# Kernel tuning notes

Hardware: AMD Instinct MI355X
Metric: run time of the kernel (lower is better)

The kernel has to match this reference:

```python
import jax, jax.numpy as jnp
import numpy as np

DIM = 1024
NUM_HEADS = 16
HEAD_DIM = DIM // NUM_HEADS


def setup_inputs() -> dict:
    key = jax.random.key(0)
    ks = jax.random.split(key, 6)
    B, N, C = 2, 2048, DIM
    s = 1.0 / np.sqrt(C)
    return {
        "x": jax.random.normal(ks[0], (B, N, C), dtype=jnp.float32),
        "Wq": jax.random.normal(ks[1], (C, C), dtype=jnp.float32) * s,
        "Wk": jax.random.normal(ks[2], (C, C), dtype=jnp.float32) * s,
        "Wv": jax.random.normal(ks[3], (C, C), dtype=jnp.float32) * s,
        "Wproj": jax.random.normal(ks[4], (C, C), dtype=jnp.float32) * s,
        "bproj": jax.random.normal(ks[5], (C,), dtype=jnp.float32) * 0.01,
    }


def reference(x, Wq, Wk, Wv, Wproj, bproj):
    B, N, C = x.shape
    H, D = NUM_HEADS, HEAD_DIM
    scale = D ** -0.5
    # Linear (torch convention: y = x @ W.T), then split heads -> [B, H, N, D]
    q = (x @ Wq.T).reshape(B, N, H, D).transpose(0, 2, 1, 3)
    k = (x @ Wk.T).reshape(B, N, H, D).transpose(0, 2, 1, 3)
    v = (x @ Wv.T).reshape(B, N, H, D).transpose(0, 2, 1, 3)
    attn = jnp.einsum("bhnd,bhmd->bhnm", q, k) * scale  # [B,H,N,N]
    attn = jax.nn.softmax(attn, axis=-1)
    out = jnp.einsum("bhnm,bhmd->bhnd", attn, v)  # [B,H,N,D]
    out = out.transpose(0, 2, 1, 3).reshape(B, N, C)
    return out @ Wproj.T + bproj
```

## Files before the change

### kernel.cpp

```cpp
#include <hip/hip_runtime.h>
#include <stdint.h>

typedef unsigned short u16;
typedef unsigned int u32;

typedef __bf16 bf16x8 __attribute__((ext_vector_type(8)));
typedef float f32x4 __attribute__((ext_vector_type(4)));

#define LOG2E_SCALE 0.18033688011112042f

static __device__ __forceinline__ u16 f2bf(float f) {
  union { float f; u32 u; } v; v.f = f;
  u32 r = v.u + 0x7fffu + ((v.u >> 16) & 1u);
  return (u16)(r >> 16);
}
static __device__ __forceinline__ u32 pk2(float a, float b) {
  return (u32)f2bf(a) | ((u32)f2bf(b) << 16);
}

static __device__ __forceinline__ void gl_lds16(const void* g, void* l) {
  __builtin_amdgcn_global_load_lds(
      (const __attribute__((address_space(1))) u32*)g,
      (__attribute__((address_space(3))) u32*)l, 16, 0, 0);
}

__global__ void cast_kernel(const float* __restrict__ x, const float* __restrict__ wq,
                            const float* __restrict__ wk, const float* __restrict__ wv,
                            const float* __restrict__ wp,
                            u16* __restrict__ xb, u16* __restrict__ wqb, u16* __restrict__ wkb,
                            u16* __restrict__ wvb, u16* __restrict__ wpb) {
  const float* src; u16* dst; int n;
  switch (blockIdx.y) {
    case 0: src = x;  dst = xb;  n = 4194304; break;
    case 1: src = wq; dst = wqb; n = 1048576; break;
    case 2: src = wk; dst = wkb; n = 1048576; break;
    case 3: src = wv; dst = wvb; n = 1048576; break;
    default: src = wp; dst = wpb; n = 1048576; break;
  }
  int i = (blockIdx.x * 256 + threadIdx.x) * 8;
  if (i >= n) return;
  float4 a = *(const float4*)(src + i);
  float4 b = *(const float4*)(src + i + 4);
  uint4 o;
  o.x = pk2(a.x, a.y); o.y = pk2(a.z, a.w);
  o.z = pk2(b.x, b.y); o.w = pk2(b.z, b.w);
  *(uint4*)(dst + i) = o;
}

__global__ __launch_bounds__(256, 3) void gemm_all(
    const u16* __restrict__ A, const u16* __restrict__ Bq, const u16* __restrict__ Bk,
    const u16* __restrict__ Bv, u16* __restrict__ oQ, u16* __restrict__ oK,
    u16* __restrict__ oVt, float* __restrict__ oP, const float* __restrict__ bias, int proj)
{
  constexpr int K = 1024;
  __shared__ u16 As[128 * 32];
  __shared__ u16 Bs[128 * 32];
  __shared__ float tbuf[4][16 * 68];

  const int tid  = threadIdx.x;
  const int lane = tid & 63;
  const int wave = tid >> 6;
  const int cl   = lane & 15;
  const int g    = lane >> 4;
  const int wm   = (wave >> 1) * 64;
  const int wn   = (wave & 1) * 64;
  const int bm   = blockIdx.y * 128;
  const int bn   = blockIdx.x * 128;
  const int z    = blockIdx.z;
  const u16* B = proj ? Bq : (z == 0 ? Bq : (z == 1 ? Bk : Bv));

  f32x4 zero4 = {0.f, 0.f, 0.f, 0.f};
  f32x4 acc[4][4];
#pragma unroll
  for (int i = 0; i < 4; i++)
#pragma unroll
    for (int j = 0; j < 4; j++) acc[i][j] = zero4;

  const int srow = tid >> 2;
  const int sch  = (tid & 3) ^ ((srow >> 1) & 3);
  const char* aG = (const char*)(A + (size_t)(bm + srow) * K) + sch * 16;
  const char* bG = (const char*)(B + (size_t)(bn + srow) * K) + sch * 16;
  char* aL = (char*)As + tid * 16;
  char* bL = (char*)Bs + tid * 16;
  const size_t rstep = (size_t)64 * K * 2;

  const int swz = (cl >> 1) & 3;

  for (int k0 = 0; k0 < K; k0 += 32) {
    gl_lds16(aG + k0 * 2, aL);
    gl_lds16(aG + rstep + k0 * 2, aL + 4096);
    gl_lds16(bG + k0 * 2, bL);
    gl_lds16(bG + rstep + k0 * 2, bL + 4096);
    __syncthreads();

    bf16x8 af[4], bf[4];
#pragma unroll
    for (int i = 0; i < 4; i++)
      af[i] = *(const bf16x8*)(As + (wm + i * 16 + cl) * 32 + ((g ^ swz) & 3) * 8);
#pragma unroll
    for (int j = 0; j < 4; j++)
      bf[j] = *(const bf16x8*)(Bs + (wn + j * 16 + cl) * 32 + ((g ^ swz) & 3) * 8);
#pragma unroll
    for (int i = 0; i < 4; i++)
#pragma unroll
      for (int j = 0; j < 4; j++)
        acc[i][j] = __builtin_amdgcn_mfma_f32_16x16x32_bf16(af[i], bf[j], acc[i][j], 0, 0, 0);
    __syncthreads();
  }

  const int rq = g * 4;
  if (proj) {
#pragma unroll
    for (int i = 0; i < 4; i++)
#pragma unroll
      for (int j = 0; j < 4; j++)
#pragma unroll
        for (int r = 0; r < 4; r++) {
          int gm = bm + wm + i * 16 + rq + r;
          int gn = bn + wn + j * 16 + cl;
          oP[(size_t)gm * 1024 + gn] = acc[i][j][r] + bias[gn];
        }
  } else if (z <= 1) {
    u16* o = z ? oK : oQ;
#pragma unroll
    for (int i = 0; i < 4; i++)
#pragma unroll
      for (int j = 0; j < 4; j++)
#pragma unroll
        for (int r = 0; r < 4; r++) {
          int gm = bm + wm + i * 16 + rq + r;
          int gn = bn + wn + j * 16 + cl;
          int b = gm >> 11, ns = gm & 2047;
          int h = gn >> 6,  d  = gn & 63;
          o[(((size_t)(b * 16 + h)) * 2048 + ns) * 64 + d] = f2bf(acc[i][j][r]);
        }
  } else {
    float* tb = tbuf[wave];
#pragma unroll
    for (int j = 0; j < 4; j++) {
      asm volatile("s_waitcnt lgkmcnt(0)" ::: "memory");
#pragma unroll
      for (int i = 0; i < 4; i++)
        *(f32x4*)(tb + cl * 68 + i * 16 + rq) = acc[i][j];
      asm volatile("s_waitcnt lgkmcnt(0)" ::: "memory");
#pragma unroll
      for (int half = 0; half < 2; half++) {
        int dd = lane >> 2, p = (lane & 3) + half * 4;
        f32x4 x0 = *(const f32x4*)(tb + dd * 68 + p * 8);
        f32x4 x1 = *(const f32x4*)(tb + dd * 68 + p * 8 + 4);
        uint4 pkd;
        pkd.x = pk2(x0[0], x0[1]); pkd.y = pk2(x0[2], x0[3]);
        pkd.z = pk2(x1[0], x1[1]); pkd.w = pk2(x1[2], x1[3]);
        int gn = bn + wn + j * 16 + dd;
        int gm = bm + wm + p * 8;
        int b = gm >> 11, nn = gm & 2047;
        int h = gn >> 6,  dl = gn & 63;
        *(uint4*)(oVt + (((size_t)(b * 16 + h)) * 64 + dl) * 2048 + nn) = pkd;
      }
    }
  }
}

__global__ __launch_bounds__(256, 2) void attn_kernel(
    const u16* __restrict__ Q, const u16* __restrict__ Km,
    const u16* __restrict__ Vt, u16* __restrict__ O)
{
  __shared__ u16 ks[128 * 64];
  __shared__ u16 ps[128 * 128];
  __shared__ u16 vs[2][64 * 128];

  const int tid  = threadIdx.x;
  const int lane = tid & 63;
  const int wave = tid >> 6;
  const int cl   = lane & 15;
  const int g    = lane >> 4;
  const int bh   = blockIdx.y;
  const int qt   = blockIdx.x;

  const char* kB = (const char*)Km + (size_t)bh * 2048 * 128;
  const char* vB = (const char*)Vt + (size_t)bh * 64 * 4096;

  const u16* qbase = Q + ((size_t)bh * 2048 + qt * 128 + wave * 32) * 64;
  bf16x8 qf[2][2];
#pragma unroll
  for (int i = 0; i < 2; i++)
#pragma unroll
    for (int h = 0; h < 2; h++)
      qf[i][h] = *(const bf16x8*)(qbase + (i * 16 + cl) * 64 + h * 32 + g * 8);

  auto stage_k = [&](int t) {
    const char* kT = kB + (size_t)t * 16384;
#pragma unroll
    for (int r = 0; r < 4; r++) {
      int c = r * 256 + tid;
      int kv = c >> 3, s = c & 7;
      gl_lds16(kT + kv * 128 + ((s ^ (kv & 7)) * 16), (char*)ks + c * 16);
    }
  };
  auto stage_v = [&](int t) {
    const char* vT = vB + (size_t)t * 256;
    char* dst = (char*)vs[t & 1];
#pragma unroll
    for (int r = 0; r < 4; r++) {
      int c = r * 256 + tid;
      int d = c >> 4, s = c & 15;
      int ch = (s & 8) | ((s ^ (d & 7)) & 7);
      gl_lds16(vT + (size_t)d * 4096 + ch * 16, dst + c * 16);
    }
  };

  stage_k(0);
  stage_v(0);

  f32x4 zero4 = {0.f, 0.f, 0.f, 0.f};
  f32x4 o_acc[2][4];
#pragma unroll
  for (int i = 0; i < 2; i++)
#pragma unroll
    for (int j = 0; j < 4; j++) o_acc[i][j] = zero4;
  float mi[2] = {-3.0e38f, -3.0e38f};
  float li[2] = {0.f, 0.f};

  for (int t = 0; t < 16; ++t) {
    __syncthreads();
    if (t < 15) stage_v(t + 1);

    f32x4 st[8][2];
#pragma unroll
    for (int j = 0; j < 8; j++) { st[j][0] = zero4; st[j][1] = zero4; }
#pragma unroll
    for (int h = 0; h < 2; h++) {
#pragma unroll
      for (int j = 0; j < 8; j++) {
        bf16x8 kf = *(const bf16x8*)(ks + (j * 16 + cl) * 64 + (((h * 4 + g) ^ (cl & 7)) & 7) * 8);
        st[j][0] = __builtin_amdgcn_mfma_f32_16x16x32_bf16(kf, qf[0][h], st[j][0], 0, 0, 0);
        st[j][1] = __builtin_amdgcn_mfma_f32_16x16x32_bf16(kf, qf[1][h], st[j][1], 0, 0, 0);
      }
    }

    float alpha[2];
#pragma unroll
    for (int i = 0; i < 2; i++) {
      float mn = -3.0e38f;
#pragma unroll
      for (int j = 0; j < 8; j++)
#pragma unroll
        for (int r = 0; r < 4; r++) mn = fmaxf(mn, st[j][i][r]);
      mn = fmaxf(mn, __shfl_xor(mn, 16, 64));
      mn = fmaxf(mn, __shfl_xor(mn, 32, 64));
      float mt = fmaxf(mi[i], mn);
      alpha[i] = exp2f((mi[i] - mt) * LOG2E_SCALE);
      mi[i] = mt;
      float rs = 0.f;
#pragma unroll
      for (int j = 0; j < 8; j++)
#pragma unroll
        for (int r = 0; r < 4; r++) {
          float p = exp2f((st[j][i][r] - mt) * LOG2E_SCALE);
          st[j][i][r] = p;
          rs += p;
        }
      rs += __shfl_xor(rs, 16, 64);
      rs += __shfl_xor(rs, 32, 64);
      li[i] = li[i] * alpha[i] + rs;
    }

#pragma unroll
    for (int i = 0; i < 2; i++)
#pragma unroll
      for (int r = 0; r < 4; r++) {
        float ar = __shfl(alpha[i], g * 4 + r, 64);
#pragma unroll
        for (int j = 0; j < 4; j++) o_acc[i][j][r] *= ar;
      }

#pragma unroll
    for (int i = 0; i < 2; i++) {
      int q = wave * 32 + i * 16 + cl;
#pragma unroll
      for (int j = 0; j < 8; j++) {
        int ch = 2 * j + (g >> 1);
        int slot = (ch & 8) | ((ch ^ (cl & 7)) & 7);
        uint2 w;
        w.x = pk2(st[j][i][0], st[j][i][1]);
        w.y = pk2(st[j][i][2], st[j][i][3]);
        *(uint2*)((char*)ps + q * 256 + slot * 16 + (g & 1) * 8) = w;
      }
    }

    __syncthreads();
    if (t < 15) stage_k(t + 1);

    const u16* vb = vs[t & 1];
#pragma unroll
    for (int ks0 = 0; ks0 < 128; ks0 += 32) {
      int c0 = ks0 >> 3;
      bf16x8 pf[2], vf[4];
#pragma unroll
      for (int i = 0; i < 2; i++) {
        int ch = c0 + g;
        int slot = (ch & 8) | ((ch ^ (cl & 7)) & 7);
        pf[i] = *(const bf16x8*)(ps + (wave * 32 + i * 16 + cl) * 128 + slot * 8);
      }
#pragma unroll
      for (int j = 0; j < 4; j++) {
        int ch = c0 + g;
        int slot = (ch & 8) | ((ch ^ (cl & 7)) & 7);
        vf[j] = *(const bf16x8*)(vb + (j * 16 + cl) * 128 + slot * 8);
      }
#pragma unroll
      for (int i = 0; i < 2; i++)
#pragma unroll
        for (int j = 0; j < 4; j++)
          o_acc[i][j] = __builtin_amdgcn_mfma_f32_16x16x32_bf16(pf[i], vf[j], o_acc[i][j], 0, 0, 0);
    }
  }

  const int b = bh >> 4, hh = bh & 15;
#pragma unroll
  for (int i = 0; i < 2; i++) {
    float inv = 1.0f / li[i];
#pragma unroll
    for (int r = 0; r < 4; r++) {
      float vr = __shfl(inv, g * 4 + r, 64);
      int row = qt * 128 + wave * 32 + i * 16 + g * 4 + r;
      u16* orow = O + ((size_t)b * 2048 + row) * 1024 + hh * 64;
#pragma unroll
      for (int j = 0; j < 4; j++)
        orow[j * 16 + cl] = f2bf(o_acc[i][j][r] * vr);
    }
  }
}

extern "C" void kernel_launch(void* const* d_in, const int* in_sizes, int n_in,
                              void* d_out, int out_size, void* d_ws, size_t ws_size,
                              hipStream_t stream) {
  const float* x     = (const float*)d_in[0];
  const float* Wq    = (const float*)d_in[1];
  const float* Wk    = (const float*)d_in[2];
  const float* Wv    = (const float*)d_in[3];
  const float* Wp    = (const float*)d_in[4];
  const float* bproj = (const float*)d_in[5];

  u16* ws  = (u16*)d_ws;
  u16* xb  = ws;
  u16* wqb = xb + 4194304;
  u16* wkb = wqb + 1048576;
  u16* wvb = wkb + 1048576;
  u16* wpb = wvb + 1048576;
  u16* Qw  = wpb + 1048576;
  u16* Kw  = Qw + 4194304;
  u16* Vw  = Kw + 4194304;
  u16* Ow  = Vw + 4194304;
  (void)in_sizes; (void)n_in; (void)out_size; (void)ws_size;

  cast_kernel<<<dim3(2048, 5), 256, 0, stream>>>(x, Wq, Wk, Wv, Wp, xb, wqb, wkb, wvb, wpb);
  gemm_all<<<dim3(8, 32, 3), 256, 0, stream>>>(xb, wqb, wkb, wvb, Qw, Kw, Vw, nullptr, nullptr, 0);
  attn_kernel<<<dim3(16, 32), 256, 0, stream>>>(Qw, Kw, Vw, Ow);
  gemm_all<<<dim3(8, 32, 1), 256, 0, stream>>>(Ow, wpb, wpb, wpb, nullptr, nullptr, nullptr,
                                               (float*)d_out, bproj, 1);
}
```

Measured before the change: 218.8 us.

## Double-buffer K tiles, drop mid-loop barrier, and use hardware bf16 pack and exp2

K tiles become double-buffered so the next K and V tiles are both prefetched at the top of each iteration. This removes the second __syncthreads per iteration. The P staging buffer is halved and P·V runs in two 64-column halves, which relies on each wave reading back only its own rows of P without a barrier. Conversions use v_cvt_pk_bf16_f32 and exp uses the raw exp2 intrinsic with a fused multiply-add. The cost is more LDS for the second K buffer and fewer instructions in the softmax and pack code.

```diff
diff --git a/kernel.cpp b/kernel.cpp
--- a/kernel.cpp
+++ b/kernel.cpp
@@ -15,7 +15,12 @@
   return (u16)(r >> 16);
 }
 static __device__ __forceinline__ u32 pk2(float a, float b) {
-  return (u32)f2bf(a) | ((u32)f2bf(b) << 16);
+  u32 r;
+  asm("v_cvt_pk_bf16_f32 %0, %1, %2" : "=v"(r) : "v"(a), "v"(b));
+  return r;
+}
+static __device__ __forceinline__ float fexp2(float x) {
+  return __builtin_amdgcn_exp2f(x);
 }
 
 static __device__ __forceinline__ void gl_lds16(const void* g, void* l) {
@@ -165,9 +170,9 @@
     const u16* __restrict__ Q, const u16* __restrict__ Km,
     const u16* __restrict__ Vt, u16* __restrict__ O)
 {
-  __shared__ u16 ks[128 * 64];
-  __shared__ u16 ps[128 * 128];
+  __shared__ u16 ks[2][128 * 64];
   __shared__ u16 vs[2][64 * 128];
+  __shared__ u16 ps[128 * 64];
 
   const int tid  = threadIdx.x;
   const int lane = tid & 63;
@@ -190,11 +195,12 @@
 
   auto stage_k = [&](int t) {
     const char* kT = kB + (size_t)t * 16384;
+    char* dst = (char*)ks[t & 1];
 #pragma unroll
     for (int r = 0; r < 4; r++) {
       int c = r * 256 + tid;
       int kv = c >> 3, s = c & 7;
-      gl_lds16(kT + kv * 128 + ((s ^ (kv & 7)) * 16), (char*)ks + c * 16);
+      gl_lds16(kT + kv * 128 + ((s ^ (kv & 7)) * 16), dst + c * 16);
     }
   };
   auto stage_v = [&](int t) {
@@ -223,7 +229,10 @@
 
   for (int t = 0; t < 16; ++t) {
     __syncthreads();
-    if (t < 15) stage_v(t + 1);
+    if (t < 15) { stage_k(t + 1); stage_v(t + 1); }
+
+    const u16* kb = ks[t & 1];
+    const u16* vb = vs[t & 1];
 
     f32x4 st[8][2];
 #pragma unroll
@@ -232,7 +241,7 @@
     for (int h = 0; h < 2; h++) {
 #pragma unroll
       for (int j = 0; j < 8; j++) {
-        bf16x8 kf = *(const bf16x8*)(ks + (j * 16 + cl) * 64 + (((h * 4 + g) ^ (cl & 7)) & 7) * 8);
+        bf16x8 kf = *(const bf16x8*)(kb + (j * 16 + cl) * 64 + (((h * 4 + g) ^ (cl & 7)) & 7) * 8);
         st[j][0] = __builtin_amdgcn_mfma_f32_16x16x32_bf16(kf, qf[0][h], st[j][0], 0, 0, 0);
         st[j][1] = __builtin_amdgcn_mfma_f32_16x16x32_bf16(kf, qf[1][h], st[j][1], 0, 0, 0);
       }
@@ -249,14 +258,15 @@
       mn = fmaxf(mn, __shfl_xor(mn, 16, 64));
       mn = fmaxf(mn, __shfl_xor(mn, 32, 64));
       float mt = fmaxf(mi[i], mn);
-      alpha[i] = exp2f((mi[i] - mt) * LOG2E_SCALE);
+      alpha[i] = fexp2((mi[i] - mt) * LOG2E_SCALE);
       mi[i] = mt;
+      float mS = mt * LOG2E_SCALE;
       float rs = 0.f;
 #pragma unroll
       for (int j = 0; j < 8; j++)
 #pragma unroll
         for (int r = 0; r < 4; r++) {
-          float p = exp2f((st[j][i][r] - mt) * LOG2E_SCALE);
+          float p = fexp2(fmaf(st[j][i][r], LOG2E_SCALE, -mS));
           st[j][i][r] = p;
           rs += p;
         }
@@ -275,44 +285,40 @@
       }
 
 #pragma unroll
-    for (int i = 0; i < 2; i++) {
-      int q = wave * 32 + i * 16 + cl;
-#pragma unroll
-      for (int j = 0; j < 8; j++) {
-        int ch = 2 * j + (g >> 1);
-        int slot = (ch & 8) | ((ch ^ (cl & 7)) & 7);
-        uint2 w;
-        w.x = pk2(st[j][i][0], st[j][i][1]);
-        w.y = pk2(st[j][i][2], st[j][i][3]);
-        *(uint2*)((char*)ps + q * 256 + slot * 16 + (g & 1) * 8) = w;
-      }
-    }
-
-    __syncthreads();
-    if (t < 15) stage_k(t + 1);
-
-    const u16* vb = vs[t & 1];
-#pragma unroll
-    for (int ks0 = 0; ks0 < 128; ks0 += 32) {
-      int c0 = ks0 >> 3;
-      bf16x8 pf[2], vf[4];
+    for (int h = 0; h < 2; h++) {
 #pragma unroll
       for (int i = 0; i < 2; i++) {
-        int ch = c0 + g;
-        int slot = (ch & 8) | ((ch ^ (cl & 7)) & 7);
-        pf[i] = *(const bf16x8*)(ps + (wave * 32 + i * 16 + cl) * 128 + slot * 8);
-      }
-#pragma unroll
-      for (int j = 0; j < 4; j++) {
-        int ch = c0 + g;
-        int slot = (ch & 8) | ((ch ^ (cl & 7)) & 7);
-        vf[j] = *(const bf16x8*)(vb + (j * 16 + cl) * 128 + slot * 8);
-      }
-#pragma unroll
-      for (int i = 0; i < 2; i++)
+        int q = wave * 32 + i * 16 + cl;
+#pragma unroll
+        for (int jj = 0; jj < 4; jj++) {
+          int j = h * 4 + jj;
+          int ch = 2 * jj + (g >> 1);
+          int slot = (ch ^ (cl & 7)) & 7;
+          uint2 w;
+          w.x = pk2(st[j][i][0], st[j][i][1]);
+          w.y = pk2(st[j][i][2], st[j][i][3]);
+          *(uint2*)((char*)ps + q * 128 + slot * 16 + (g & 1) * 8) = w;
+        }
+      }
+#pragma unroll
+      for (int kb32 = 0; kb32 < 2; kb32++) {
+        int chp = kb32 * 4 + g;
+        int slotp = (chp ^ (cl & 7)) & 7;
+        int chv = h * 8 + kb32 * 4 + g;
+        int slotv = (chv & 8) | ((chv ^ (cl & 7)) & 7);
+        bf16x8 pf[2], vf[4];
+#pragma unroll
+        for (int i = 0; i < 2; i++)
+          pf[i] = *(const bf16x8*)((const char*)ps + (wave * 32 + i * 16 + cl) * 128 + slotp * 16);
 #pragma unroll
         for (int j = 0; j < 4; j++)
-          o_acc[i][j] = __builtin_amdgcn_mfma_f32_16x16x32_bf16(pf[i], vf[j], o_acc[i][j], 0, 0, 0);
+          vf[j] = *(const bf16x8*)((const char*)vb + (j * 16 + cl) * 256 + slotv * 16);
+#pragma unroll
+        for (int i = 0; i < 2; i++)
+#pragma unroll
+          for (int j = 0; j < 4; j++)
+            o_acc[i][j] = __builtin_amdgcn_mfma_f32_16x16x32_bf16(pf[i], vf[j], o_acc[i][j], 0, 0, 0);
+      }
     }
   }
 
```

After: 194.1 us. 1.13x faster.
